# Performance work log

Hardware: AMD Instinct MI355X
Metric: run time of the kernel (lower is better)

Reference implementation:

```python
import jax, jax.numpy as jnp
import numpy as np

N_NODES = 50000
N_EDGES = 800000
HEADS = 4
OUT_C = 64
NEG_SLOPE = 0.2


def setup_inputs() -> dict:
    key = jax.random.key(0)
    k1, k2, k3, k4 = jax.random.split(key, 4)
    x = jax.random.normal(k1, (N_NODES, OUT_C), dtype=jnp.float32)
    edge_index = jax.random.randint(k2, (2, N_EDGES), 0, N_NODES, dtype=jnp.int64)
    # Glorot-ish scaling for stability
    W = jax.random.normal(k3, (OUT_C, HEADS * OUT_C), dtype=jnp.float32) * (1.0 / np.sqrt(OUT_C))
    att = jax.random.normal(k4, (HEADS, OUT_C), dtype=jnp.float32) * (1.0 / np.sqrt(OUT_C))
    bias = jnp.zeros((HEADS * OUT_C,), dtype=jnp.float32)
    return {"x": x, "edge_index": edge_index, "W": W, "att": att, "bias": bias}


def _gatv2(x, edge_index, W, att, bias):
    N = x.shape[0]
    src, dst = edge_index[0], edge_index[1]
    # shared weights: x_l == x_r
    xl = (x @ W).reshape(N, HEADS, OUT_C)  # [N,H,C]
    feat = xl[src] + xl[dst]               # [E,H,C] per-edge gather
    feat = jnp.where(feat > 0, feat, NEG_SLOPE * feat)  # LeakyReLU
    score = jnp.einsum('ehc,hc->eh', feat, att)          # [E,H]
    # segment softmax over destination nodes
    smax = jax.ops.segment_max(score, dst, num_segments=N)  # [N,H]
    smax = jnp.where(jnp.isfinite(smax), smax, 0.0)
    ex = jnp.exp(score - smax[dst])                          # [E,H]
    denom = jax.ops.segment_sum(ex, dst, num_segments=N)     # [N,H]
    denom = jnp.where(denom > 0, denom, 1.0)
    alpha = ex / denom[dst]                                  # [E,H]
    msg = alpha[:, :, None] * xl[src]                        # [E,H,C]
    out = jax.ops.segment_sum(msg, dst, num_segments=N)      # [N,H,C]
    out = out.reshape(N, HEADS * OUT_C) + bias
    return jax.nn.relu(out)


def reference(x, edge_index, W, att, bias):
    return _gatv2(x, edge_index, W, att, bias)
```

## Files before the change

### kernel.cpp

```cpp
#include <hip/hip_runtime.h>
#include <math.h>

#define N_NODES 50000
#define N_EDGES 800000
#define HEADS 4
#define OUT_C 64
#define HC 256
#define NEG_SLOPE 0.2f
#define NBUCKET 196
#define CHUNK 1000
#define NBLK 800
#define WT_BLOCKS 64
#define GEMM_BLOCKS (N_NODES / 16)
#define LOG2E 1.44269504f

typedef __attribute__((ext_vector_type(8))) short bf16x8;
typedef __attribute__((ext_vector_type(4))) float f32x4;

__device__ inline unsigned short f2bf(float f) {
    unsigned u = __float_as_uint(f);
    return (unsigned short)((u + 0x7FFFu + ((u >> 16) & 1u)) >> 16);
}

__device__ inline float ub0(unsigned q) { return (float)(q & 0xFFu); }
__device__ inline float ub1(unsigned q) { return (float)((q >> 8) & 0xFFu); }
__device__ inline float ub2(unsigned q) { return (float)((q >> 16) & 0xFFu); }
__device__ inline float ub3(unsigned q) { return (float)(q >> 24); }

__device__ inline float rowsum16(float p) {
    int y;
    y = __builtin_amdgcn_update_dpp(0, __float_as_int(p), 0x121, 0xF, 0xF, false);
    p += __int_as_float(y);
    y = __builtin_amdgcn_update_dpp(0, __float_as_int(p), 0x122, 0xF, 0xF, false);
    p += __int_as_float(y);
    y = __builtin_amdgcn_update_dpp(0, __float_as_int(p), 0x124, 0xF, 0xF, false);
    p += __int_as_float(y);
    y = __builtin_amdgcn_update_dpp(0, __float_as_int(p), 0x128, 0xF, 0xF, false);
    p += __int_as_float(y);
    return p;
}

__global__ void k_hist1(const int* __restrict__ dst, int* __restrict__ M,
                        const float* __restrict__ W, unsigned short* __restrict__ Wt,
                        int* __restrict__ done) {
    int b = blockIdx.x, t = threadIdx.x;
    if (b >= NBLK) {
        if (b == NBLK && t == 0) *done = 0;
        int idx = (b - NBLK) * 256 + t;
        int c = idx >> 6, k = idx & 63;
        Wt[idx] = f2bf(W[(size_t)k * HC + c]);
        return;
    }
    __shared__ int h[NBUCKET];
    if (t < NBUCKET) h[t] = 0;
    __syncthreads();
    int base = b * CHUNK;
    for (int i = base + t; i < base + CHUNK; i += 256)
        atomicAdd(&h[dst[i] >> 8], 1);
    __syncthreads();
    if (t < NBUCKET) M[(size_t)t * NBLK + b] = h[t];
}

__global__ void k_scan2(int* __restrict__ M, int* __restrict__ coarse,
                        int* __restrict__ coarseBase, int* __restrict__ rowL,
                        int* __restrict__ ssorted, int* __restrict__ done) {
    __shared__ int wsum[4];
    __shared__ int carry_s, tot_s, lastflag;
    int b = blockIdx.x, t = threadIdx.x;
    int lane = t & 63, w = t >> 6;
    if (t == 0) carry_s = 0;
    __syncthreads();
    int* Mrow = M + (size_t)b * NBLK;
    for (int c0 = 0; c0 < NBLK; c0 += 256) {
        int idx = c0 + t;
        int v = (idx < NBLK) ? Mrow[idx] : 0;
        int x = v;
        #pragma unroll
        for (int off = 1; off < 64; off <<= 1) {
            int y = __shfl_up(x, off);
            if (lane >= off) x += y;
        }
        if (lane == 63) wsum[w] = x;
        __syncthreads();
        if (t == 0) {
            int s0 = wsum[0], s1 = wsum[1], s2 = wsum[2], s3 = wsum[3];
            wsum[0] = 0; wsum[1] = s0; wsum[2] = s0 + s1; wsum[3] = s0 + s1 + s2;
            tot_s = s0 + s1 + s2 + s3;
        }
        __syncthreads();
        int excl = x - v + wsum[w] + carry_s;
        if (idx < NBLK) Mrow[idx] = excl;
        __syncthreads();
        if (t == 0) carry_s += tot_s;
        __syncthreads();
    }
    if (t == 0) coarse[b] = carry_s;
    __threadfence();
    if (t == 0) lastflag = (atomicAdd(done, 1) == NBUCKET - 1);
    __syncthreads();
    if (!lastflag) return;
    if (t == 0) *done = 0;
    __threadfence();
    int v = (t < NBUCKET) ? coarse[t] : 0;
    int x = v;
    #pragma unroll
    for (int off = 1; off < 64; off <<= 1) {
        int y = __shfl_up(x, off);
        if (lane >= off) x += y;
    }
    if (lane == 63) wsum[w] = x;
    __syncthreads();
    if (t == 0) {
        int s0 = wsum[0], s1 = wsum[1], s2 = wsum[2];
        wsum[0] = 0; wsum[1] = s0; wsum[2] = s0 + s1; wsum[3] = s0 + s1 + s2;
    }
    __syncthreads();
    int excl = x - v + wsum[w];
    if (t < NBUCKET) coarseBase[t] = excl;
    if (t == NBUCKET - 1) coarseBase[NBUCKET] = excl + v;
    if (t == 0) rowL[N_NODES] = N_EDGES;
    if (t < 16) ssorted[N_EDGES + t] = 0;
}

__global__ __launch_bounds__(256) void k_scatter_gemm(
    const int* __restrict__ src, const int* __restrict__ dst,
    const int* __restrict__ M, const int* __restrict__ coarseBase,
    int* __restrict__ tmp,
    const float* __restrict__ x, const unsigned short* __restrict__ Wt,
    unsigned char* __restrict__ xq, float* __restrict__ scl) {
    __shared__ int shmem[NBUCKET];
    int b = blockIdx.x, t = threadIdx.x;
    if (b < NBLK) {
        int* cur = shmem;
        if (t < NBUCKET) cur[t] = coarseBase[t] + M[(size_t)t * NBLK + b];
        __syncthreads();
        int base = b * CHUNK;
        for (int i = base + t; i < base + CHUNK; i += 256) {
            int d = dst[i];
            int pos = atomicAdd(&cur[d >> 8], 1);
            tmp[pos] = ((d & 255) << 16) | src[i];
        }
        return;
    }
    int* rmax = shmem;
    int wv = t >> 6, l = t & 63;
    int row0 = (b - NBLK) * 16;
    int r = l & 15, kg = l >> 4, ko = kg * 8;
    const float* xrow = x + (size_t)(row0 + r) * OUT_C;
    f32x4 a0 = *(const f32x4*)(xrow + ko);
    f32x4 a1 = *(const f32x4*)(xrow + ko + 4);
    f32x4 a2 = *(const f32x4*)(xrow + 32 + ko);
    f32x4 a3 = *(const f32x4*)(xrow + 32 + ko + 4);
    bf16x8 A0, A1;
    #pragma unroll
    for (int j = 0; j < 4; ++j) {
        A0[j]     = (short)f2bf(a0[j]);
        A0[j + 4] = (short)f2bf(a1[j]);
        A1[j]     = (short)f2bf(a2[j]);
        A1[j + 4] = (short)f2bf(a3[j]);
    }
    if (t < 16) rmax[t] = __float_as_int(1e-6f);
    __syncthreads();
    f32x4 acc0 = {0,0,0,0}, acc1 = {0,0,0,0}, acc2 = {0,0,0,0}, acc3 = {0,0,0,0};
#define DO_TILE(ACC, I) {                                                     \
        const unsigned short* wp = Wt + (size_t)(wv * 16 + (I) * 64 + r) * OUT_C + ko; \
        bf16x8 B0 = *(const bf16x8*)(wp);                                     \
        bf16x8 B1 = *(const bf16x8*)(wp + 32);                                \
        ACC = __builtin_amdgcn_mfma_f32_16x16x32_bf16(A0, B0, ACC, 0, 0, 0);  \
        ACC = __builtin_amdgcn_mfma_f32_16x16x32_bf16(A1, B1, ACC, 0, 0, 0); }
    DO_TILE(acc0, 0) DO_TILE(acc1, 1) DO_TILE(acc2, 2) DO_TILE(acc3, 3)
#undef DO_TILE
    int drow = kg * 4;
    #pragma unroll
    for (int j = 0; j < 4; ++j) {
        float m = fmaxf(fmaxf(fabsf(acc0[j]), fabsf(acc1[j])),
                        fmaxf(fabsf(acc2[j]), fabsf(acc3[j])));
        atomicMax(&rmax[drow + j], __float_as_int(m));
    }
    __syncthreads();
    float is[4];
    #pragma unroll
    for (int j = 0; j < 4; ++j)
        is[j] = 127.0f / __int_as_float(rmax[drow + j]);
    #pragma unroll
    for (int j = 0; j < 4; ++j) {
        size_t base = (size_t)(row0 + drow + j) * HC + r;
        xq[base + wv * 16 + 0 * 64] = (unsigned char)((int)rintf(acc0[j] * is[j]) + 128);
        xq[base + wv * 16 + 1 * 64] = (unsigned char)((int)rintf(acc1[j] * is[j]) + 128);
        xq[base + wv * 16 + 2 * 64] = (unsigned char)((int)rintf(acc2[j] * is[j]) + 128);
        xq[base + wv * 16 + 3 * 64] = (unsigned char)((int)rintf(acc3[j] * is[j]) + 128);
    }
    if (t < 16) scl[row0 + t] = __int_as_float(rmax[t]) * (1.0f / 127.0f);
}

__global__ void k_csr(const int* __restrict__ tmp, const int* __restrict__ coarseBase,
                      int* __restrict__ rowL, int* __restrict__ ssorted) {
    __shared__ int h[256];
    __shared__ int cur[256];
    __shared__ int wsum[4];
    int b = blockIdx.x, t = threadIdx.x;
    int lane = t & 63, w = t >> 6;
    int s = coarseBase[b], e = coarseBase[b + 1];
    h[t] = 0;
    __syncthreads();
    for (int i = s + t; i < e; i += 256)
        atomicAdd(&h[(tmp[i] >> 16) & 255], 1);
    __syncthreads();
    int v = h[t];
    int x = v;
    #pragma unroll
    for (int off = 1; off < 64; off <<= 1) {
        int y = __shfl_up(x, off);
        if (lane >= off) x += y;
    }
    if (lane == 63) wsum[w] = x;
    __syncthreads();
    if (t == 0) {
        int s0 = wsum[0], s1 = wsum[1], s2 = wsum[2];
        wsum[0] = 0; wsum[1] = s0; wsum[2] = s0 + s1; wsum[3] = s0 + s1 + s2;
    }
    __syncthreads();
    int excl = x - v + wsum[w];
    int n = b * 256 + t;
    if (n < N_NODES) rowL[n] = s + excl;
    cur[t] = s + excl;
    __syncthreads();
    for (int i = s + t; i < e; i += 256) {
        int p = tmp[i];
        int pos = atomicAdd(&cur[(p >> 16) & 255], 1);
        ssorted[pos] = p & 0xFFFF;
    }
}

__global__ __launch_bounds__(256) void k_node(
    const unsigned char* __restrict__ xq, const float* __restrict__ scl,
    const int* __restrict__ rowL, const int* __restrict__ ssorted,
    const float* __restrict__ att, const float* __restrict__ bias,
    float* __restrict__ out) {
    int w = threadIdx.x >> 6;
    int lane = threadIdx.x & 63;
    int n = blockIdx.x * 4 + w;
    int start = __builtin_amdgcn_readfirstlane(rowL[n]);
    int end   = __builtin_amdgcn_readfirstlane(rowL[n + 1]);
    int ne = end - start;
    const int* sp = ssorted + start;
    int c4 = lane << 2;
    const unsigned char* xp = xq + c4;
    float sn = scl[n];
    float offn = 128.0f * sn;
    unsigned qn = *(const unsigned*)(xp + (size_t)n * HC);
    float4 xn;
    xn.x = ub0(qn) * sn - offn;
    xn.y = ub1(qn) * sn - offn;
    xn.z = ub2(qn) * sn - offn;
    xn.w = ub3(qn) * sn - offn;
    float4 at = *(const float4*)(att + c4);
    float4 at6 = make_float4(at.x * (0.6f * LOG2E), at.y * (0.6f * LOG2E),
                             at.z * (0.6f * LOG2E), at.w * (0.6f * LOG2E));
    float4 at4 = make_float4(at.x * (0.4f * LOG2E), at.y * (0.4f * LOG2E),
                             at.z * (0.4f * LOG2E), at.w * (0.4f * LOG2E));
    float4 accf = make_float4(0.f, 0.f, 0.f, 0.f);
    float den = 0.0f;

#define EDGE(qv, sv) {                                                    \
        float xo_x = xn.x - 128.0f * sv, xo_y = xn.y - 128.0f * sv;       \
        float xo_z = xn.z - 128.0f * sv, xo_w = xn.w - 128.0f * sv;       \
        float f0 = ub0(qv) * sv + xo_x;                                   \
        float f1 = ub1(qv) * sv + xo_y;                                   \
        float f2 = ub2(qv) * sv + xo_z;                                   \
        float f3 = ub3(qv) * sv + xo_w;                                   \
        float p;                                                          \
        p  = f0 * at6.x + fabsf(f0) * at4.x;                              \
        p += f1 * at6.y + fabsf(f1) * at4.y;                              \
        p += f2 * at6.z + fabsf(f2) * at4.z;                              \
        p += f3 * at6.w + fabsf(f3) * at4.w;                              \
        p = rowsum16(p);                                                  \
        float ex = exp2f(p);                                              \
        den += ex;                                                        \
        accf.x += ex * f0; accf.y += ex * f1;                             \
        accf.z += ex * f2; accf.w += ex * f3; }

    if (ne > 0) {
        int sa = sp[0];
        int sb = sp[1];
        unsigned qa = *(const unsigned*)(xp + (size_t)sa * HC);
        unsigned qb = *(const unsigned*)(xp + (size_t)sb * HC);
        float ssa = scl[sa], ssb = scl[sb];
        sa = sp[2];
        sb = sp[3];
        int i = 0;
        for (; i + 1 < ne; i += 2) {
            unsigned q0 = qa, q1 = qb;
            float s0 = ssa, s1 = ssb;
            qa = *(const unsigned*)(xp + (size_t)sa * HC);
            qb = *(const unsigned*)(xp + (size_t)sb * HC);
            ssa = scl[sa]; ssb = scl[sb];
            sa = sp[i + 4];
            sb = sp[i + 5];
            EDGE(q0, s0);
            EDGE(q1, s1);
        }
        if (i < ne) EDGE(qa, ssa);
    }
#undef EDGE

    float r = 1.0f / (den > 0.0f ? den : 1.0f);
    float4 b4 = *(const float4*)(bias + c4);
    float4 o;
    o.x = fmaxf((accf.x - xn.x * den) * r + b4.x, 0.0f);
    o.y = fmaxf((accf.y - xn.y * den) * r + b4.y, 0.0f);
    o.z = fmaxf((accf.z - xn.z * den) * r + b4.z, 0.0f);
    o.w = fmaxf((accf.w - xn.w * den) * r + b4.w, 0.0f);
    *(float4*)(out + (size_t)n * HC + c4) = o;
}

extern "C" void kernel_launch(void* const* d_in, const int* in_sizes, int n_in,
                              void* d_out, int out_size, void* d_ws, size_t ws_size,
                              hipStream_t stream) {
    const float* x    = (const float*)d_in[0];
    const int*   edge = (const int*)d_in[1];
    const float* W    = (const float*)d_in[2];
    const float* att  = (const float*)d_in[3];
    const float* bias = (const float*)d_in[4];
    float* out = (float*)d_out;

    const int* src = edge;
    const int* dst = edge + N_EDGES;

    char* ws = (char*)d_ws;
    unsigned char* xq  = (unsigned char*)ws;
    float* scl      = (float*)(ws + 12800000);
    unsigned short* Wt = (unsigned short*)(ws + 13000000);
    int* M          = (int*)(ws + 13032768);
    int* coarse     = (int*)(ws + 13659968);
    int* coarseBase = (int*)(ws + 13660800);
    int* done       = (int*)(ws + 13661632);
    int* rowL       = (int*)(ws + 13661696);
    int* tmp        = (int*)(ws + 13861760);
    int* ssorted    = (int*)(ws + 17061760);

    k_hist1<<<NBLK + WT_BLOCKS, 256, 0, stream>>>(dst, M, W, Wt, done);
    k_scan2<<<NBUCKET, 256, 0, stream>>>(M, coarse, coarseBase, rowL, ssorted, done);
    k_scatter_gemm<<<NBLK + GEMM_BLOCKS, 256, 0, stream>>>(src, dst, M, coarseBase,
                                                           tmp, x, Wt, xq, scl);
    k_csr<<<NBUCKET, 256, 0, stream>>>(tmp, coarseBase, rowL, ssorted);
    k_node<<<N_NODES / 4, 256, 0, stream>>>(xq, scl, rowL, ssorted, att, bias, out);
}
```

Measured before the change: 131.2 us.

## Merge preprocessing kernels using intra-kernel spin-wait flags instead of launches

```diff
diff --git a/kernel.cpp b/kernel.cpp
--- a/kernel.cpp
+++ b/kernel.cpp
@@ -11,7 +11,8 @@
 #define CHUNK 1000
 #define NBLK 800
 #define WT_BLOCKS 64
-#define GEMM_BLOCKS (N_NODES / 16)
+#define GEMM_BLOCKS 3125
+#define GEMM_WORKERS 256
 #define LOG2E 1.44269504f
 
 typedef __attribute__((ext_vector_type(8))) short bf16x8;
@@ -40,47 +41,56 @@
     return p;
 }
 
-__global__ void k_hist1(const int* __restrict__ dst, int* __restrict__ M,
-                        const float* __restrict__ W, unsigned short* __restrict__ Wt,
-                        int* __restrict__ done) {
+__device__ inline void spin_until(int* flag, int target) {
+    while (__hip_atomic_load(flag, __ATOMIC_RELAXED, __HIP_MEMORY_SCOPE_AGENT) < target)
+        __builtin_amdgcn_s_sleep(2);
+}
+
+__global__ __launch_bounds__(256) void k_build1(
+    const int* __restrict__ dst, int* __restrict__ M,
+    const float* __restrict__ W, unsigned short* __restrict__ Wt,
+    int* __restrict__ coarse, int* __restrict__ coarseBase,
+    int* __restrict__ rowL, int* __restrict__ ssorted, int* __restrict__ flags) {
     int b = blockIdx.x, t = threadIdx.x;
-    if (b >= NBLK) {
-        if (b == NBLK && t == 0) *done = 0;
+    int lane = t & 63, w = t >> 6;
+
+    if (b < NBLK) {
+        __shared__ int h[NBUCKET];
+        if (t < NBUCKET) h[t] = 0;
+        __syncthreads();
+        int base = b * CHUNK;
+        for (int i = base + t; i < base + CHUNK; i += 256)
+            atomicAdd(&h[dst[i] >> 8], 1);
+        __syncthreads();
+        if (t < NBUCKET) M[(size_t)t * NBLK + b] = h[t];
+        __threadfence();
+        __syncthreads();
+        if (t == 0) atomicAdd(&flags[0], 1);
+        return;
+    }
+    if (b < NBLK + WT_BLOCKS) {
         int idx = (b - NBLK) * 256 + t;
         int c = idx >> 6, k = idx & 63;
         Wt[idx] = f2bf(W[(size_t)k * HC + c]);
         return;
     }
-    __shared__ int h[NBUCKET];
-    if (t < NBUCKET) h[t] = 0;
-    __syncthreads();
-    int base = b * CHUNK;
-    for (int i = base + t; i < base + CHUNK; i += 256)
-        atomicAdd(&h[dst[i] >> 8], 1);
-    __syncthreads();
-    if (t < NBUCKET) M[(size_t)t * NBLK + b] = h[t];
-}
-
-__global__ void k_scan2(int* __restrict__ M, int* __restrict__ coarse,
-                        int* __restrict__ coarseBase, int* __restrict__ rowL,
-                        int* __restrict__ ssorted, int* __restrict__ done) {
     __shared__ int wsum[4];
     __shared__ int carry_s, tot_s, lastflag;
-    int b = blockIdx.x, t = threadIdx.x;
-    int lane = t & 63, w = t >> 6;
-    if (t == 0) carry_s = 0;
-    __syncthreads();
-    int* Mrow = M + (size_t)b * NBLK;
+    int sb = b - NBLK - WT_BLOCKS;
+    if (t == 0) { spin_until(&flags[0], NBLK); carry_s = 0; }
+    __syncthreads();
+    __threadfence();
+    int* Mrow = M + (size_t)sb * NBLK;
     for (int c0 = 0; c0 < NBLK; c0 += 256) {
         int idx = c0 + t;
         int v = (idx < NBLK) ? Mrow[idx] : 0;
-        int x = v;
+        int xs = v;
         #pragma unroll
         for (int off = 1; off < 64; off <<= 1) {
-            int y = __shfl_up(x, off);
-            if (lane >= off) x += y;
-        }
-        if (lane == 63) wsum[w] = x;
+            int y = __shfl_up(xs, off);
+            if (lane >= off) xs += y;
+        }
+        if (lane == 63) wsum[w] = xs;
         __syncthreads();
         if (t == 0) {
             int s0 = wsum[0], s1 = wsum[1], s2 = wsum[2], s3 = wsum[3];
@@ -88,48 +98,50 @@
             tot_s = s0 + s1 + s2 + s3;
         }
         __syncthreads();
-        int excl = x - v + wsum[w] + carry_s;
+        int excl = xs - v + wsum[w] + carry_s;
         if (idx < NBLK) Mrow[idx] = excl;
         __syncthreads();
         if (t == 0) carry_s += tot_s;
         __syncthreads();
     }
-    if (t == 0) coarse[b] = carry_s;
+    if (t == 0) coarse[sb] = carry_s;
     __threadfence();
-    if (t == 0) lastflag = (atomicAdd(done, 1) == NBUCKET - 1);
+    if (t == 0) lastflag = (atomicAdd(&flags[1], 1) == NBUCKET - 1);
     __syncthreads();
     if (!lastflag) return;
-    if (t == 0) *done = 0;
     __threadfence();
     int v = (t < NBUCKET) ? coarse[t] : 0;
-    int x = v;
+    int xs = v;
     #pragma unroll
     for (int off = 1; off < 64; off <<= 1) {
-        int y = __shfl_up(x, off);
-        if (lane >= off) x += y;
-    }
-    if (lane == 63) wsum[w] = x;
+        int y = __shfl_up(xs, off);
+        if (lane >= off) xs += y;
+    }
+    if (lane == 63) wsum[w] = xs;
     __syncthreads();
     if (t == 0) {
         int s0 = wsum[0], s1 = wsum[1], s2 = wsum[2];
         wsum[0] = 0; wsum[1] = s0; wsum[2] = s0 + s1; wsum[3] = s0 + s1 + s2;
     }
     __syncthreads();
-    int excl = x - v + wsum[w];
+    int excl = xs - v + wsum[w];
     if (t < NBUCKET) coarseBase[t] = excl;
     if (t == NBUCKET - 1) coarseBase[NBUCKET] = excl + v;
     if (t == 0) rowL[N_NODES] = N_EDGES;
     if (t < 16) ssorted[N_EDGES + t] = 0;
 }
 
-__global__ __launch_bounds__(256) void k_scatter_gemm(
+__global__ __launch_bounds__(256) void k_build2(
     const int* __restrict__ src, const int* __restrict__ dst,
     const int* __restrict__ M, const int* __restrict__ coarseBase,
     int* __restrict__ tmp,
-    const float* __restrict__ x, const unsigned short* __restrict__ Wt,
-    unsigned char* __restrict__ xq, float* __restrict__ scl) {
-    __shared__ int shmem[NBUCKET];
+    const float* __restrict__ xf, const unsigned short* __restrict__ Wt,
+    unsigned char* __restrict__ xq, float* __restrict__ scl,
+    int* __restrict__ rowL, int* __restrict__ ssorted, int* __restrict__ flags) {
+    __shared__ int shmem[520];
     int b = blockIdx.x, t = threadIdx.x;
+    int lane = t & 63, w = t >> 6;
+
     if (b < NBLK) {
         int* cur = shmem;
         if (t < NBUCKET) cur[t] = coarseBase[t] + M[(size_t)t * NBLK + b];
@@ -140,88 +152,96 @@
             int pos = atomicAdd(&cur[d >> 8], 1);
             tmp[pos] = ((d & 255) << 16) | src[i];
         }
+        __threadfence();
+        __syncthreads();
+        if (t == 0) atomicAdd(&flags[2], 1);
         return;
     }
-    int* rmax = shmem;
-    int wv = t >> 6, l = t & 63;
-    int row0 = (b - NBLK) * 16;
-    int r = l & 15, kg = l >> 4, ko = kg * 8;
-    const float* xrow = x + (size_t)(row0 + r) * OUT_C;
-    f32x4 a0 = *(const f32x4*)(xrow + ko);
-    f32x4 a1 = *(const f32x4*)(xrow + ko + 4);
-    f32x4 a2 = *(const f32x4*)(xrow + 32 + ko);
-    f32x4 a3 = *(const f32x4*)(xrow + 32 + ko + 4);
-    bf16x8 A0, A1;
-    #pragma unroll
-    for (int j = 0; j < 4; ++j) {
-        A0[j]     = (short)f2bf(a0[j]);
-        A0[j + 4] = (short)f2bf(a1[j]);
-        A1[j]     = (short)f2bf(a2[j]);
-        A1[j + 4] = (short)f2bf(a3[j]);
-    }
-    if (t < 16) rmax[t] = __float_as_int(1e-6f);
-    __syncthreads();
-    f32x4 acc0 = {0,0,0,0}, acc1 = {0,0,0,0}, acc2 = {0,0,0,0}, acc3 = {0,0,0,0};
+    if (b < NBLK + GEMM_WORKERS) {
+        int* rmax = shmem;
+        int g = b - NBLK;
+        int wv = t >> 6, l = t & 63;
+        int r = l & 15, kg = l >> 4, ko = kg * 8;
+        int drow = kg * 4;
+        for (int rg = g; rg < GEMM_BLOCKS; rg += GEMM_WORKERS) {
+            int row0 = rg * 16;
+            const float* xrow = xf + (size_t)(row0 + r) * OUT_C;
+            f32x4 a0 = *(const f32x4*)(xrow + ko);
+            f32x4 a1 = *(const f32x4*)(xrow + ko + 4);
+            f32x4 a2 = *(const f32x4*)(xrow + 32 + ko);
+            f32x4 a3 = *(const f32x4*)(xrow + 32 + ko + 4);
+            bf16x8 A0, A1;
+            #pragma unroll
+            for (int j = 0; j < 4; ++j) {
+                A0[j]     = (short)f2bf(a0[j]);
+                A0[j + 4] = (short)f2bf(a1[j]);
+                A1[j]     = (short)f2bf(a2[j]);
+                A1[j + 4] = (short)f2bf(a3[j]);
+            }
+            if (t < 16) rmax[t] = __float_as_int(1e-6f);
+            __syncthreads();
+            f32x4 acc0 = {0,0,0,0}, acc1 = {0,0,0,0}, acc2 = {0,0,0,0}, acc3 = {0,0,0,0};
 #define DO_TILE(ACC, I) {                                                     \
-        const unsigned short* wp = Wt + (size_t)(wv * 16 + (I) * 64 + r) * OUT_C + ko; \
-        bf16x8 B0 = *(const bf16x8*)(wp);                                     \
-        bf16x8 B1 = *(const bf16x8*)(wp + 32);                                \
-        ACC = __builtin_amdgcn_mfma_f32_16x16x32_bf16(A0, B0, ACC, 0, 0, 0);  \
-        ACC = __builtin_amdgcn_mfma_f32_16x16x32_bf16(A1, B1, ACC, 0, 0, 0); }
-    DO_TILE(acc0, 0) DO_TILE(acc1, 1) DO_TILE(acc2, 2) DO_TILE(acc3, 3)
+            const unsigned short* wp = Wt + (size_t)(wv * 16 + (I) * 64 + r) * OUT_C + ko; \
+            bf16x8 B0 = *(const bf16x8*)(wp);                                 \
+            bf16x8 B1 = *(const bf16x8*)(wp + 32);                            \
+            ACC = __builtin_amdgcn_mfma_f32_16x16x32_bf16(A0, B0, ACC, 0, 0, 0); \
+            ACC = __builtin_amdgcn_mfma_f32_16x16x32_bf16(A1, B1, ACC, 0, 0, 0); }
+            DO_TILE(acc0, 0) DO_TILE(acc1, 1) DO_TILE(acc2, 2) DO_TILE(acc3, 3)
 #undef DO_TILE
-    int drow = kg * 4;
-    #pragma unroll
-    for (int j = 0; j < 4; ++j) {
-        float m = fmaxf(fmaxf(fabsf(acc0[j]), fabsf(acc1[j])),
-                        fmaxf(fabsf(acc2[j]), fabsf(acc3[j])));
-        atomicMax(&rmax[drow + j], __float_as_int(m));
-    }
-    __syncthreads();
-    float is[4];
-    #pragma unroll
-    for (int j = 0; j < 4; ++j)
-        is[j] = 127.0f / __int_as_float(rmax[drow + j]);
-    #pragma unroll
-    for (int j = 0; j < 4; ++j) {
-        size_t base = (size_t)(row0 + drow + j) * HC + r;
-        xq[base + wv * 16 + 0 * 64] = (unsigned char)((int)rintf(acc0[j] * is[j]) + 128);
-        xq[base + wv * 16 + 1 * 64] = (unsigned char)((int)rintf(acc1[j] * is[j]) + 128);
-        xq[base + wv * 16 + 2 * 64] = (unsigned char)((int)rintf(acc2[j] * is[j]) + 128);
-        xq[base + wv * 16 + 3 * 64] = (unsigned char)((int)rintf(acc3[j] * is[j]) + 128);
-    }
-    if (t < 16) scl[row0 + t] = __int_as_float(rmax[t]) * (1.0f / 127.0f);
-}
-
-__global__ void k_csr(const int* __restrict__ tmp, const int* __restrict__ coarseBase,
-                      int* __restrict__ rowL, int* __restrict__ ssorted) {
-    __shared__ int h[256];
-    __shared__ int cur[256];
-    __shared__ int wsum[4];
-    int b = blockIdx.x, t = threadIdx.x;
-    int lane = t & 63, w = t >> 6;
-    int s = coarseBase[b], e = coarseBase[b + 1];
+            #pragma unroll
+            for (int j = 0; j < 4; ++j) {
+                float m = fmaxf(fmaxf(fabsf(acc0[j]), fabsf(acc1[j])),
+                                fmaxf(fabsf(acc2[j]), fabsf(acc3[j])));
+                atomicMax(&rmax[drow + j], __float_as_int(m));
+            }
+            __syncthreads();
+            float is[4];
+            #pragma unroll
+            for (int j = 0; j < 4; ++j)
+                is[j] = 127.0f / __int_as_float(rmax[drow + j]);
+            #pragma unroll
+            for (int j = 0; j < 4; ++j) {
+                size_t base = (size_t)(row0 + drow + j) * HC + r;
+                xq[base + wv * 16 + 0 * 64] = (unsigned char)((int)rintf(acc0[j] * is[j]) + 128);
+                xq[base + wv * 16 + 1 * 64] = (unsigned char)((int)rintf(acc1[j] * is[j]) + 128);
+                xq[base + wv * 16 + 2 * 64] = (unsigned char)((int)rintf(acc2[j] * is[j]) + 128);
+                xq[base + wv * 16 + 3 * 64] = (unsigned char)((int)rintf(acc3[j] * is[j]) + 128);
+            }
+            if (t < 16) scl[row0 + t] = __int_as_float(rmax[t]) * (1.0f / 127.0f);
+            __syncthreads();
+        }
+        return;
+    }
+    int* h    = shmem;
+    int* cur  = shmem + 256;
+    int* wsum = shmem + 512;
+    int cb = b - NBLK - GEMM_WORKERS;
+    if (t == 0) spin_until(&flags[2], NBLK);
+    __syncthreads();
+    __threadfence();
+    int s = coarseBase[cb], e = coarseBase[cb + 1];
     h[t] = 0;
     __syncthreads();
     for (int i = s + t; i < e; i += 256)
         atomicAdd(&h[(tmp[i] >> 16) & 255], 1);
     __syncthreads();
     int v = h[t];
-    int x = v;
+    int xs = v;
     #pragma unroll
     for (int off = 1; off < 64; off <<= 1) {
-        int y = __shfl_up(x, off);
-        if (lane >= off) x += y;
-    }
-    if (lane == 63) wsum[w] = x;
+        int y = __shfl_up(xs, off);
+        if (lane >= off) xs += y;
+    }
+    if (lane == 63) wsum[w] = xs;
     __syncthreads();
     if (t == 0) {
         int s0 = wsum[0], s1 = wsum[1], s2 = wsum[2];
         wsum[0] = 0; wsum[1] = s0; wsum[2] = s0 + s1; wsum[3] = s0 + s1 + s2;
     }
     __syncthreads();
-    int excl = x - v + wsum[w];
-    int n = b * 256 + t;
+    int excl = xs - v + wsum[w];
+    int n = cb * 256 + t;
     if (n < N_NODES) rowL[n] = s + excl;
     cur[t] = s + excl;
     __syncthreads();
@@ -334,15 +354,15 @@
     int* M          = (int*)(ws + 13032768);
     int* coarse     = (int*)(ws + 13659968);
     int* coarseBase = (int*)(ws + 13660800);
-    int* done       = (int*)(ws + 13661632);
+    int* flags      = (int*)(ws + 13661632);
     int* rowL       = (int*)(ws + 13661696);
     int* tmp        = (int*)(ws + 13861760);
     int* ssorted    = (int*)(ws + 17061760);
 
-    k_hist1<<<NBLK + WT_BLOCKS, 256, 0, stream>>>(dst, M, W, Wt, done);
-    k_scan2<<<NBUCKET, 256, 0, stream>>>(M, coarse, coarseBase, rowL, ssorted, done);
-    k_scatter_gemm<<<NBLK + GEMM_BLOCKS, 256, 0, stream>>>(src, dst, M, coarseBase,
-                                                           tmp, x, Wt, xq, scl);
-    k_csr<<<NBUCKET, 256, 0, stream>>>(tmp, coarseBase, rowL, ssorted);
+    (void)hipMemsetAsync(flags, 0, 64, stream);
+    k_build1<<<NBLK + WT_BLOCKS + NBUCKET, 256, 0, stream>>>(
+        dst, M, W, Wt, coarse, coarseBase, rowL, ssorted, flags);
+    k_build2<<<NBLK + GEMM_WORKERS + NBUCKET, 256, 0, stream>>>(
+        src, dst, M, coarseBase, tmp, x, Wt, xq, scl, rowL, ssorted, flags);
     k_node<<<N_NODES / 4, 256, 0, stream>>>(xq, scl, rowL, ssorted, att, bias, out);
 }
```

Result: slower. 399.4 us (+204.4%).
